# Optimization experiments

Hardware: AMD Instinct MI355X
Metric: run time of the kernel (lower is better)

The kernel has to match this reference:

```python
import jax, jax.numpy as jnp
import numpy as np

NEG_BIG = -9e15
ALPHA = 0.2  # LeakyReLU negative slope
B, N, F_IN, F_OUT = 8, 2048, 128, 128


def setup_inputs() -> dict:
    key = jax.random.key(0)
    k1, k2, k3, k4 = jax.random.split(key, 4)
    inp = jax.random.normal(k1, (B, N, F_IN), dtype=jnp.float32)
    adj = jax.random.randint(k2, (B, N, N), 0, 2, dtype=jnp.int32)
    W = 0.02 * jax.random.normal(k3, (F_OUT, F_IN), dtype=jnp.float32)  # nn.Linear weight [out,in]
    a = 0.02 * jax.random.normal(k4, (1, 2 * F_OUT), dtype=jnp.float32)  # attention vector [1, 2F]
    return {"input": inp, "adj": adj, "W": W, "a": a}


def reference(input, adj, W, a):
    # h = input @ W^T : [B, N, F_OUT]
    h = jnp.einsum("bnf,of->bno", input, W)
    f_out = h.shape[-1]
    # Decompose a . [h_i || h_j] = (h_i . a1) + (h_j . a2) -- same math as the
    # explicit repeat_interleave/repeat/cat, without the O(N^2 * 2F) tensor.
    a1 = a[0, :f_out]
    a2 = a[0, f_out:]
    s1 = h @ a1  # [B, N] score for source node i
    s2 = h @ a2  # [B, N] score for target node j
    e = jax.nn.leaky_relu(s1[:, :, None] + s2[:, None, :], negative_slope=ALPHA)  # [B,N,N]
    masked = jnp.where(adj > 0, e, NEG_BIG)
    attention = jax.nn.softmax(masked, axis=-1)
    # dropout p=0.0 (eval) -> identity
    h_prime = jnp.einsum("bnm,bmo->bno", attention, h)
    return h_prime
```

## Files before the change

### kernel.cpp

```cpp
#include <hip/hip_runtime.h>
#include <stdint.h>


#define B_ 8
#define N_ 2048
#define FD 128
#define ALPHA_ 0.2f
#define TJ 64
#define NCHL 16
#define CHUNK_U4 1024

typedef __attribute__((ext_vector_type(8))) short short8;
typedef __attribute__((ext_vector_type(4))) float f32x4;

#define HCHUNK(o, jc) ((((o) * 16) + ((jc) ^ ((o) & 15))) * 8)
#define HC64(o, jc) ((o) * 8 + ((jc) ^ ((o) & 7)))

__device__ __forceinline__ float bf2f(unsigned short u) {
    union { uint32_t i; float f; } v; v.i = ((uint32_t)u) << 16; return v.f;
}
__device__ __forceinline__ unsigned short f2bf(float f) {
    union { float f; uint32_t i; } v; v.f = f;
    uint32_t x = v.i;
    uint32_t r = (x + 0x7fffu + ((x >> 16) & 1u)) >> 16;
    return (unsigned short)r;
}

__device__ __forceinline__ void gl2lds16(const uint4* g, uint4* l) {
    __builtin_amdgcn_global_load_lds(
        (const __attribute__((address_space(1))) uint32_t*)g,
        (__attribute__((address_space(3))) uint32_t*)l, 16, 0, 0);
}

__global__ __launch_bounds__(256) void gat_h(
    const float* __restrict__ x,
    const float* __restrict__ W,
    const float* __restrict__ a,
    unsigned short* __restrict__ hT,
    float* __restrict__ s1o, float* __restrict__ s2o)
{
    __shared__ __align__(16) unsigned short Wlds[FD * FD];

    const int bid = blockIdx.x;
    const int tid = threadIdx.x;
    const int w = tid >> 6;
    const int lane = tid & 63;
    const int m = lane & 15;
    const int quad = lane >> 4;
    const int arow = bid * 64 + w * 16 + m;

#pragma unroll
    for (int it = 0; it < 8; it++) {
        int cid = it * 256 + tid;
        int o = cid >> 4, kc = cid & 15;
        const float* wp = W + (size_t)o * FD + kc * 8;
        float4 w0 = *(const float4*)wp;
        float4 w1 = *(const float4*)(wp + 4);
        uint4 pk;
        pk.x = (uint32_t)f2bf(w0.x) | ((uint32_t)f2bf(w0.y) << 16);
        pk.y = (uint32_t)f2bf(w0.z) | ((uint32_t)f2bf(w0.w) << 16);
        pk.z = (uint32_t)f2bf(w1.x) | ((uint32_t)f2bf(w1.y) << 16);
        pk.w = (uint32_t)f2bf(w1.z) | ((uint32_t)f2bf(w1.w) << 16);
        *(uint4*)&Wlds[HCHUNK(o, kc)] = pk;
    }
    __syncthreads();

    f32x4 acc[8];
#pragma unroll
    for (int ot = 0; ot < 8; ot++) acc[ot] = (f32x4){0.f, 0.f, 0.f, 0.f};

#pragma unroll
    for (int ks = 0; ks < 4; ks++) {
        const float* xp = x + (size_t)arow * FD + ks * 32 + quad * 8;
        float4 x0 = *(const float4*)xp;
        float4 x1 = *(const float4*)(xp + 4);
        float xv[8] = {x0.x, x0.y, x0.z, x0.w, x1.x, x1.y, x1.z, x1.w};
        union { unsigned short us[8]; short8 v; } ahi, alo;
#pragma unroll
        for (int jj = 0; jj < 8; jj++) {
            unsigned short hi = f2bf(xv[jj]);
            ahi.us[jj] = hi;
            alo.us[jj] = f2bf(xv[jj] - bf2f(hi));
        }
#pragma unroll
        for (int ot = 0; ot < 8; ot++) {
            union { uint4 u; short8 v; } bw;
            bw.u = *(const uint4*)&Wlds[HCHUNK(ot * 16 + m, ks * 4 + quad)];
            acc[ot] = __builtin_amdgcn_mfma_f32_16x16x32_bf16(ahi.v, bw.v, acc[ot], 0, 0, 0);
            acc[ot] = __builtin_amdgcn_mfma_f32_16x16x32_bf16(alo.v, bw.v, acc[ot], 0, 0, 0);
        }
    }

    const int rc0 = bid * 64 + w * 16 + quad * 4;
    const int bb = rc0 >> 11;
    const int jb = rc0 & (N_ - 1);
    const int kc = jb >> 6;
    const int jcl = (jb & 63) >> 3;
    const int off = jb & 7;
    unsigned short* hTb = hT + (size_t)bb * FD * N_ + (size_t)kc * (CHUNK_U4 * 8);
    float s1p[4] = {0.f, 0.f, 0.f, 0.f};
    float s2p[4] = {0.f, 0.f, 0.f, 0.f};
#pragma unroll
    for (int ot = 0; ot < 8; ot++) {
        const int o = ot * 16 + m;
        uint2 pk;
        pk.x = (uint32_t)f2bf(acc[ot][0]) | ((uint32_t)f2bf(acc[ot][1]) << 16);
        pk.y = (uint32_t)f2bf(acc[ot][2]) | ((uint32_t)f2bf(acc[ot][3]) << 16);
        *(uint2*)(hTb + (size_t)HC64(o, jcl) * 8 + off) = pk;
        float a1v = a[o], a2v = a[FD + o];
#pragma unroll
        for (int r = 0; r < 4; r++) {
            s1p[r] += acc[ot][r] * a1v;
            s2p[r] += acc[ot][r] * a2v;
        }
    }
#pragma unroll
    for (int offx = 8; offx >= 1; offx >>= 1) {
#pragma unroll
        for (int r = 0; r < 4; r++) {
            s1p[r] += __shfl_xor(s1p[r], offx);
            s2p[r] += __shfl_xor(s2p[r], offx);
        }
    }
    if (m == 0) {
#pragma unroll
        for (int r = 0; r < 4; r++) {
            s1o[rc0 + r] = s1p[r];
            s2o[rc0 + r] = s2p[r];
        }
    }
}

__global__ __launch_bounds__(256, 2) void gat_attn(
    const int* __restrict__ adj,
    const unsigned short* __restrict__ hT,
    const float* __restrict__ s1,
    const float* __restrict__ s2,
    float* __restrict__ out)
{
    __shared__ __align__(16) uint4 hbuf[2][2][CHUNK_U4];

    const int bid = blockIdx.x;
    const int b = bid >> 6;
    const int i0 = (bid & 63) * 32;
    const int tid = threadIdx.x;
    const int lane = tid & 63;
    const int w = tid >> 6;
    const int jh = w >> 1;
    const int rh = w & 1;
    const int m = lane & 15;
    const int quad = lane >> 4;

    const int irow = i0 + rh * 16 + m;
    const float s1v = s1[b * N_ + irow];
    const int* adjrow = adj + ((size_t)(b * N_ + irow)) * N_ + jh * 1024;
    const uint4* hTc = (const uint4*)(hT + (size_t)b * FD * N_)
                       + (size_t)jh * NCHL * CHUNK_U4;
    const float* s2b = s2 + b * N_ + jh * 1024;

#pragma unroll
    for (int it = 0; it < 8; it++)
        gl2lds16(&hTc[it * 128 + rh * 64 + lane], &hbuf[jh][0][it * 128 + rh * 64]);
    int4 acur[4];
    float4 scur[4];
#pragma unroll
    for (int ks = 0; ks < 2; ks++) {
        acur[2 * ks]     = *(const int4*)(adjrow + ks * 32 + quad * 8);
        acur[2 * ks + 1] = *(const int4*)(adjrow + ks * 32 + quad * 8 + 4);
        scur[2 * ks]     = *(const float4*)(s2b + ks * 32 + quad * 8);
        scur[2 * ks + 1] = *(const float4*)(s2b + ks * 32 + quad * 8 + 4);
    }
    __syncthreads();

    f32x4 acc[8];
#pragma unroll
    for (int ot = 0; ot < 8; ot++) acc[ot] = (f32x4){0.f, 0.f, 0.f, 0.f};
    float rs_loc = 0.f;

    for (int k = 0; k < NCHL; k++) {
        const int buf = k & 1;
        const bool more = (k + 1 < NCHL);
        int4 anext[4];
        float4 snext[4];
        if (more) {
#pragma unroll
            for (int it = 0; it < 8; it++)
                gl2lds16(&hTc[(size_t)(k + 1) * CHUNK_U4 + it * 128 + rh * 64 + lane],
                         &hbuf[jh][buf ^ 1][it * 128 + rh * 64]);
            const int j1 = (k + 1) * TJ;
#pragma unroll
            for (int ks = 0; ks < 2; ks++) {
                anext[2 * ks]     = *(const int4*)(adjrow + j1 + ks * 32 + quad * 8);
                anext[2 * ks + 1] = *(const int4*)(adjrow + j1 + ks * 32 + quad * 8 + 4);
                snext[2 * ks]     = *(const float4*)(s2b + j1 + ks * 32 + quad * 8);
                snext[2 * ks + 1] = *(const float4*)(s2b + j1 + ks * 32 + quad * 8 + 4);
            }
        }

#pragma unroll
        for (int ks = 0; ks < 2; ks++) {
            float4 sa = scur[2 * ks], sb = scur[2 * ks + 1];
            float sarr[8] = {sa.x, sa.y, sa.z, sa.w, sb.x, sb.y, sb.z, sb.w};
            int4 A0 = acur[2 * ks], A1 = acur[2 * ks + 1];
            int aarr[8] = {A0.x, A0.y, A0.z, A0.w, A1.x, A1.y, A1.z, A1.w};
            union { unsigned short us[8]; short8 v; } af;
#pragma unroll
            for (int jj = 0; jj < 8; jj++) {
                float e = s1v + sarr[jj];
                e = (e > 0.f) ? e : (ALPHA_ * e);
                float p = (aarr[jj] > 0) ? __expf(e) : 0.f;
                rs_loc += p;
                af.us[jj] = f2bf(p);
            }
            const int jc = ks * 4 + quad;
#pragma unroll
            for (int ot = 0; ot < 8; ot++) {
                const int o = ot * 16 + m;
                union { uint4 u; short8 v; } bf;
                bf.u = *(const uint4*)&hbuf[jh][buf][HC64(o, jc)];
                acc[ot] = __builtin_amdgcn_mfma_f32_16x16x32_bf16(af.v, bf.v, acc[ot], 0, 0, 0);
            }
        }

        __syncthreads();
        if (more) {
#pragma unroll
            for (int q = 0; q < 4; q++) { acur[q] = anext[q]; scur[q] = snext[q]; }
        }
    }

    float* xch = (float*)&hbuf[0][0][0];
    rs_loc += __shfl_xor(rs_loc, 16);
    rs_loc += __shfl_xor(rs_loc, 32);
    if (jh == 1) {
#pragma unroll
        for (int ot = 0; ot < 8; ot++)
#pragma unroll
            for (int r = 0; r < 4; r++)
                xch[rh * 2048 + (quad * 4 + r) * 128 + ot * 16 + m] = acc[ot][r];
        if (quad == 0) xch[4096 + rh * 16 + m] = rs_loc;
    }
    __syncthreads();
    if (jh == 0) {
        float rinv[4];
#pragma unroll
        for (int r = 0; r < 4; r++) {
            const int p = quad * 4 + r;
            rinv[r] = 1.0f / (__shfl(rs_loc, p) + xch[4096 + rh * 16 + p]);
        }
        float* outp = out + (size_t)(b * N_ + i0 + rh * 16) * FD;
#pragma unroll
        for (int ot = 0; ot < 8; ot++) {
            const int col = ot * 16 + m;
#pragma unroll
            for (int r = 0; r < 4; r++) {
                float v = acc[ot][r] + xch[rh * 2048 + (quad * 4 + r) * 128 + col];
                outp[(size_t)(quad * 4 + r) * FD + col] = v * rinv[r];
            }
        }
    }
}

extern "C" void kernel_launch(void* const* d_in, const int* in_sizes, int n_in,
                              void* d_out, int out_size, void* d_ws, size_t ws_size,
                              hipStream_t stream) {
    const void* xv = d_in[0];
    const void* adjv = d_in[1];
    const void* Wv = d_in[2];
    const void* av = d_in[3];
    for (int i = 0; i < n_in; i++) {
        switch (in_sizes[i]) {
            case 2097152:  xv = d_in[i]; break;
            case 33554432: adjv = d_in[i]; break;
            case 16384:    Wv = d_in[i]; break;
            case 256:      av = d_in[i]; break;
            default: break;
        }
    }
    const float* x = (const float*)xv;
    const int* adj = (const int*)adjv;
    const float* W = (const float*)Wv;
    const float* a = (const float*)av;
    float* out = (float*)d_out;

    char* p = (char*)d_ws;
    unsigned short* hT = (unsigned short*)p;  p += (size_t)B_ * FD * N_ * 2;
    float* s1 = (float*)p;                    p += (size_t)B_ * N_ * 4;
    float* s2 = (float*)p;

    gat_h<<<256, 256, 0, stream>>>(x, W, a, hT, s1, s2);
    gat_attn<<<512, 256, 0, stream>>>(adj, hT, s1, s2, out);
}
```

Baseline: 217.0 us.

## Use 64-row blocks with 8 waves sharing each staged hT chunk

The attention kernel now processes 64 query rows per block with 512 threads (8 waves) instead of 32 rows with 256 threads. Each staged hT chunk in LDS is therefore reused by twice as many rows, which halves the redundant hT traffic from global memory. Block IDs are interleaved across batches, and the s2 prefetch registers are replaced by direct loads inside the loop to reduce register pressure. The grid shrinks to 256 blocks, which may lower occupancy or load balance, and the s2 loads are no longer prefetched.

```diff
diff --git a/kernel.cpp b/kernel.cpp
--- a/kernel.cpp
+++ b/kernel.cpp
@@ -131,7 +131,7 @@
     }
 }
 
-__global__ __launch_bounds__(256, 2) void gat_attn(
+__global__ __launch_bounds__(512, 4) void gat_attn(
     const int* __restrict__ adj,
     const unsigned short* __restrict__ hT,
     const float* __restrict__ s1,
@@ -141,17 +141,17 @@
     __shared__ __align__(16) uint4 hbuf[2][2][CHUNK_U4];
 
     const int bid = blockIdx.x;
-    const int b = bid >> 6;
-    const int i0 = (bid & 63) * 32;
+    const int b = bid & 7;
+    const int i0 = (bid >> 3) * 64;
     const int tid = threadIdx.x;
     const int lane = tid & 63;
     const int w = tid >> 6;
-    const int jh = w >> 1;
-    const int rh = w & 1;
+    const int jh = w >> 2;
+    const int rg = w & 3;
     const int m = lane & 15;
     const int quad = lane >> 4;
 
-    const int irow = i0 + rh * 16 + m;
+    const int irow = i0 + rg * 16 + m;
     const float s1v = s1[b * N_ + irow];
     const int* adjrow = adj + ((size_t)(b * N_ + irow)) * N_ + jh * 1024;
     const uint4* hTc = (const uint4*)(hT + (size_t)b * FD * N_)
@@ -159,16 +159,13 @@
     const float* s2b = s2 + b * N_ + jh * 1024;
 
 #pragma unroll
-    for (int it = 0; it < 8; it++)
-        gl2lds16(&hTc[it * 128 + rh * 64 + lane], &hbuf[jh][0][it * 128 + rh * 64]);
+    for (int it = 0; it < 4; it++)
+        gl2lds16(&hTc[it * 256 + rg * 64 + lane], &hbuf[jh][0][it * 256 + rg * 64]);
     int4 acur[4];
-    float4 scur[4];
 #pragma unroll
     for (int ks = 0; ks < 2; ks++) {
         acur[2 * ks]     = *(const int4*)(adjrow + ks * 32 + quad * 8);
         acur[2 * ks + 1] = *(const int4*)(adjrow + ks * 32 + quad * 8 + 4);
-        scur[2 * ks]     = *(const float4*)(s2b + ks * 32 + quad * 8);
-        scur[2 * ks + 1] = *(const float4*)(s2b + ks * 32 + quad * 8 + 4);
     }
     __syncthreads();
 
@@ -181,25 +178,23 @@
         const int buf = k & 1;
         const bool more = (k + 1 < NCHL);
         int4 anext[4];
-        float4 snext[4];
         if (more) {
 #pragma unroll
-            for (int it = 0; it < 8; it++)
-                gl2lds16(&hTc[(size_t)(k + 1) * CHUNK_U4 + it * 128 + rh * 64 + lane],
-                         &hbuf[jh][buf ^ 1][it * 128 + rh * 64]);
+            for (int it = 0; it < 4; it++)
+                gl2lds16(&hTc[(size_t)(k + 1) * CHUNK_U4 + it * 256 + rg * 64 + lane],
+                         &hbuf[jh][buf ^ 1][it * 256 + rg * 64]);
             const int j1 = (k + 1) * TJ;
 #pragma unroll
             for (int ks = 0; ks < 2; ks++) {
                 anext[2 * ks]     = *(const int4*)(adjrow + j1 + ks * 32 + quad * 8);
                 anext[2 * ks + 1] = *(const int4*)(adjrow + j1 + ks * 32 + quad * 8 + 4);
-                snext[2 * ks]     = *(const float4*)(s2b + j1 + ks * 32 + quad * 8);
-                snext[2 * ks + 1] = *(const float4*)(s2b + j1 + ks * 32 + quad * 8 + 4);
             }
         }
 
 #pragma unroll
         for (int ks = 0; ks < 2; ks++) {
-            float4 sa = scur[2 * ks], sb = scur[2 * ks + 1];
+            float4 sa = *(const float4*)(s2b + k * TJ + ks * 32 + quad * 8);
+            float4 sb = *(const float4*)(s2b + k * TJ + ks * 32 + quad * 8 + 4);
             float sarr[8] = {sa.x, sa.y, sa.z, sa.w, sb.x, sb.y, sb.z, sb.w};
             int4 A0 = acur[2 * ks], A1 = acur[2 * ks + 1];
             int aarr[8] = {A0.x, A0.y, A0.z, A0.w, A1.x, A1.y, A1.z, A1.w};
@@ -225,7 +220,7 @@
         __syncthreads();
         if (more) {
 #pragma unroll
-            for (int q = 0; q < 4; q++) { acur[q] = anext[q]; scur[q] = snext[q]; }
+            for (int q = 0; q < 4; q++) acur[q] = anext[q];
         }
     }
 
@@ -237,8 +232,8 @@
         for (int ot = 0; ot < 8; ot++)
 #pragma unroll
             for (int r = 0; r < 4; r++)
-                xch[rh * 2048 + (quad * 4 + r) * 128 + ot * 16 + m] = acc[ot][r];
-        if (quad == 0) xch[4096 + rh * 16 + m] = rs_loc;
+                xch[(rg * 16 + quad * 4 + r) * 128 + ot * 16 + m] = acc[ot][r];
+        if (quad == 0) xch[8192 + rg * 16 + m] = rs_loc;
     }
     __syncthreads();
     if (jh == 0) {
@@ -246,15 +241,15 @@
 #pragma unroll
         for (int r = 0; r < 4; r++) {
             const int p = quad * 4 + r;
-            rinv[r] = 1.0f / (__shfl(rs_loc, p) + xch[4096 + rh * 16 + p]);
-        }
-        float* outp = out + (size_t)(b * N_ + i0 + rh * 16) * FD;
+            rinv[r] = 1.0f / (__shfl(rs_loc, p) + xch[8192 + rg * 16 + p]);
+        }
+        float* outp = out + (size_t)(b * N_ + i0 + rg * 16) * FD;
 #pragma unroll
         for (int ot = 0; ot < 8; ot++) {
             const int col = ot * 16 + m;
 #pragma unroll
             for (int r = 0; r < 4; r++) {
-                float v = acc[ot][r] + xch[rh * 2048 + (quad * 4 + r) * 128 + col];
+                float v = acc[ot][r] + xch[(rg * 16 + quad * 4 + r) * 128 + col];
                 outp[(size_t)(quad * 4 + r) * FD + col] = v * rinv[r];
             }
         }
@@ -289,5 +284,5 @@
     float* s2 = (float*)p;
 
     gat_h<<<256, 256, 0, stream>>>(x, W, a, hT, s1, s2);
-    gat_attn<<<512, 256, 0, stream>>>(adj, hT, s1, s2, out);
-}
+    gat_attn<<<256, 512, 0, stream>>>(adj, hT, s1, s2, out);
+}
```

Result: slower. 226.6 us (+4.4%).
